# Optimization experiments

Hardware: AMD Instinct MI355X
Metric: run time of the kernel (lower is better)

Reference implementation:

```python
import jax, jax.numpy as jnp
import numpy as np

N, E, D, L, G = 100000, 300000, 256, 5, 4096


def _bn(x, p):
    # p: [4, dim] = (gamma, beta, running_mean, running_var); eval-mode BatchNorm1d
    g, b, m, v = p
    return (x - m) * jax.lax.rsqrt(v + 1e-5) * g + b


def setup_inputs() -> dict:
    key = jax.random.key(0)
    ks = iter(jax.random.split(key, 48))

    def nrm(shape, scale=0.02):
        return jax.random.normal(next(ks), shape, dtype=jnp.float32) * scale

    def bn_params(n, dim):
        g = 1.0 + nrm((n, dim), 0.1)
        b = nrm((n, dim), 0.1)
        m = nrm((n, dim), 0.1)
        v = 1.0 + jax.random.uniform(next(ks), (n, dim), dtype=jnp.float32)
        return jnp.stack([g, b, m, v], axis=1)  # [n,4,dim]

    return {
        "x": jax.random.randint(next(ks), (N, 9), 0, 2, dtype=jnp.int32),
        "edge_index": jax.random.randint(next(ks), (2, E), 0, N, dtype=jnp.int32),
        "edge_attr": jax.random.randint(next(ks), (E, 3), 0, 2, dtype=jnp.int32),
        "batch": jnp.sort(jax.random.randint(next(ks), (N,), 0, G, dtype=jnp.int32)),
        "atom_emb": nrm((9, 120, D)),            # AtomEncoder: 9 feature tables
        "bond_emb": nrm((L, 3, 6, D)),           # per-layer BondEncoder: 3 feature tables
        "vn0": jnp.zeros((D,), jnp.float32),     # virtualnode embedding (init 0)
        "eps": jnp.zeros((L,), jnp.float32),     # GIN eps per layer
        "conv_W1": nrm((L, D, 2 * D), 1.0 / np.sqrt(D)),     # GIN MLP (sampled BayesLinear)
        "conv_b1": nrm((L, 2 * D)),
        "conv_bn1": bn_params(L, 2 * D),
        "conv_W2": nrm((L, 2 * D, D), 1.0 / np.sqrt(2 * D)),
        "conv_b2": nrm((L, D)),
        "node_bn": bn_params(L, D),              # per-layer outer BatchNorm
        "vn_W1": nrm((L - 1, D, D), 1.0 / np.sqrt(D)),       # virtual-node MLP
        "vn_b1": nrm((L - 1, D)),
        "vn_bn1": bn_params(L - 1, D),
        "vn_W2": nrm((L - 1, D, D), 1.0 / np.sqrt(D)),
        "vn_b2": nrm((L - 1, D)),
        "vn_bn2": bn_params(L - 1, D),
    }


def reference(x, edge_index, edge_attr, batch, atom_emb, bond_emb, vn0, eps,
              conv_W1, conv_b1, conv_bn1, conv_W2, conv_b2, node_bn,
              vn_W1, vn_b1, vn_bn1, vn_W2, vn_b2, vn_bn2):
    src, dst = edge_index[0], edge_index[1]
    n_nodes = x.shape[0]
    n_layers = conv_W1.shape[0]
    # AtomEncoder: sum of 9 feature embeddings -> [N, D]
    h = atom_emb[jnp.arange(9), x].sum(axis=1)
    vn = jnp.broadcast_to(vn0, (G, vn0.shape[0]))  # [G, D]
    for l in range(n_layers):
        # broadcast virtual node into graph's nodes
        h = h + vn[batch]
        # GINConv: msg = relu(x_j + bond_emb), sum-aggregate, MLP((1+eps)x + aggr)
        e = bond_emb[l][jnp.arange(3), edge_attr].sum(axis=1)  # [E, D]
        msg = jax.nn.relu(h[src] + e)
        aggr = jax.ops.segment_sum(msg, dst, num_segments=n_nodes)
        t = (1.0 + eps[l]) * h + aggr
        t = jax.nn.relu(_bn(t @ conv_W1[l] + conv_b1[l], conv_bn1[l])) @ conv_W2[l] + conv_b2[l]
        hn = _bn(t, node_bn[l])  # outer BatchNorm (eval); dropout is identity in eval
        if l < n_layers - 1:
            hn = jax.nn.relu(hn)
            # global_add_pool of pre-conv h, then virtual-node MLP update
            vtemp = jax.ops.segment_sum(h, batch, num_segments=G) + vn
            u = jax.nn.relu(_bn(vtemp @ vn_W1[l] + vn_b1[l], vn_bn1[l]))
            vn = jax.nn.relu(_bn(u @ vn_W2[l] + vn_b2[l], vn_bn2[l]))
        h = hn
    return h  # JK == 'last'
```

## Files before the change

kernel.cpp:

```cpp
#include <hip/hip_runtime.h>

#define NN 100000
#define EE 300000
#define DD 256
#define LL 5
#define GG 4096
#define DB 512
#define MPAD 100096

typedef __attribute__((ext_vector_type(4))) float f32x4;
typedef __attribute__((ext_vector_type(8))) short s16x8;

__device__ __forceinline__ ushort f2bf(float f) {
  unsigned u = __float_as_uint(f);
  return (ushort)((u + 0x7fffu + ((u >> 16) & 1u)) >> 16);
}
__device__ __forceinline__ float b2f(ushort u) {
  return __uint_as_float(((unsigned)u) << 16);
}

__device__ __forceinline__ void gload16(const void* g, void* l) {
  __builtin_amdgcn_global_load_lds((const __attribute__((address_space(1))) void*)g,
                                   (__attribute__((address_space(3))) void*)l, 16, 0, 0);
}

__global__ void k_atom(const int* __restrict__ x, const float* __restrict__ emb,
                       const float* __restrict__ vn0, ushort* __restrict__ hvb) {
  int n = blockIdx.x * 4 + (threadIdx.x >> 6);
  if (n >= NN) return;
  int d = (threadIdx.x & 63) * 4;
  const float4 v0 = *(const float4*)&vn0[d];
  float ax = v0.x, ay = v0.y, az = v0.z, aw = v0.w;
#pragma unroll
  for (int f = 0; f < 9; ++f) {
    int v = x[n * 9 + f];
    const float4 t = *(const float4*)&emb[((size_t)(f * 120 + v)) * DD + d];
    ax += t.x; ay += t.y; az += t.z; aw += t.w;
  }
  ushort4 o; o.x = f2bf(ax); o.y = f2bf(ay); o.z = f2bf(az); o.w = f2bf(aw);
  *(ushort4*)&hvb[(size_t)n * DD + d] = o;
}

__global__ void k_vninit(const float* __restrict__ vn0, float* __restrict__ vn) {
  int i = blockIdx.x * blockDim.x + threadIdx.x;
  if (i < GG * DD) vn[i] = vn0[i & (DD - 1)];
}

__global__ void k_goff(const int* __restrict__ batch, int* __restrict__ goff) {
  int g = blockIdx.x * blockDim.x + threadIdx.x;
  if (g > GG) return;
  if (g == GG) { goff[GG] = NN; return; }
  int lo = 0, hi = NN;
  while (lo < hi) { int mid = (lo + hi) >> 1; if (batch[mid] < g) lo = mid + 1; else hi = mid; }
  goff[g] = lo;
}

__global__ void k_zero(int* __restrict__ p, int n) {
  int i = blockIdx.x * 256 + threadIdx.x;
  if (i < n) p[i] = 0;
}

__global__ void k_deg(const int* __restrict__ dst, int* __restrict__ deg) {
  int e = blockIdx.x * 256 + threadIdx.x;
  if (e < EE) atomicAdd(&deg[dst[e]], 1);
}

__global__ void k_scan1(const int* __restrict__ deg, int* __restrict__ coff,
                        int* __restrict__ bsum) {
  __shared__ int wsum[16];
  __shared__ int wpre[16];
  int lane = threadIdx.x & 63, wid = threadIdx.x >> 6;
  int i = blockIdx.x * 1024 + threadIdx.x;
  int v = (i < NN) ? deg[i] : 0;
  int xv = v;
#pragma unroll
  for (int off = 1; off < 64; off <<= 1) {
    int y = __shfl_up(xv, off);
    if (lane >= off) xv += y;
  }
  if (lane == 63) wsum[wid] = xv;
  __syncthreads();
  if (wid == 0 && lane < 16) {
    int s = wsum[lane];
    int xx = s;
#pragma unroll
    for (int off = 1; off < 16; off <<= 1) {
      int y = __shfl_up(xx, off);
      if (lane >= off) xx += y;
    }
    wpre[lane] = xx - s;
  }
  __syncthreads();
  int val = xv + wpre[wid];
  if (i < NN) coff[i + 1] = val;
  if (threadIdx.x == 1023) bsum[blockIdx.x] = val;
}

__global__ void k_scan2(int* __restrict__ bsum, int nb) {
  __shared__ int ws[2];
  int t = threadIdx.x, lane = t & 63, wid = t >> 6;
  int v = (t < nb) ? bsum[t] : 0;
  int xv = v;
#pragma unroll
  for (int off = 1; off < 64; off <<= 1) {
    int y = __shfl_up(xv, off);
    if (lane >= off) xv += y;
  }
  if (lane == 63) ws[wid] = xv;
  __syncthreads();
  int incl = xv + ((wid == 1) ? ws[0] : 0);
  if (t < nb) bsum[t] = incl - v;
}

__global__ void k_scan3(int* __restrict__ coff, const int* __restrict__ bpre) {
  int i = blockIdx.x * 1024 + threadIdx.x;
  if (i == 0) coff[0] = 0;
  if (i < NN) coff[i + 1] += bpre[i >> 10];
}

__global__ void k_eposinit(const int* __restrict__ coff, int* __restrict__ epos) {
  int n = blockIdx.x * 256 + threadIdx.x;
  if (n < NN) epos[n] = coff[n];
}

__global__ void k_scatter(const int* __restrict__ dst, int* __restrict__ epos,
                          int* __restrict__ eid) {
  int e = blockIdx.x * 256 + threadIdx.x;
  if (e < EE) { int p = atomicAdd(&epos[dst[e]], 1); eid[p] = e; }
}

__global__ void k_sort(const int* __restrict__ coff, int* __restrict__ eid) {
  int n = blockIdx.x * 256 + threadIdx.x;
  if (n >= NN) return;
  int s = coff[n], t = coff[n + 1];
  for (int i = s + 1; i < t; ++i) {
    int key = eid[i]; int j = i - 1;
    while (j >= s && eid[j] > key) { eid[j + 1] = eid[j]; --j; }
    eid[j + 1] = key;
  }
}

__global__ void k_emeta(const int* __restrict__ eid, const int* __restrict__ srcs,
                        const int* __restrict__ eattr, unsigned* __restrict__ emeta) {
  int idx = blockIdx.x * 256 + threadIdx.x;
  if (idx >= EE) return;
  int e = eid[idx];
  int s = srcs[e];
  unsigned c = (unsigned)(eattr[e * 3 + 0] + 2 * eattr[e * 3 + 1] + 4 * eattr[e * 3 + 2]);
  emeta[idx] = (unsigned)s | (c << 17);
}

__global__ void k_bond8(const float* __restrict__ bondE, float* __restrict__ bond8) {
  int l = blockIdx.x, c = blockIdx.y, d = threadIdx.x;
  float v = bondE[(((size_t)l * 3 + 0) * 6 + (c & 1)) * DD + d]
          + bondE[(((size_t)l * 3 + 1) * 6 + ((c >> 1) & 1)) * DD + d]
          + bondE[(((size_t)l * 3 + 2) * 6 + ((c >> 2) & 1)) * DD + d];
  bond8[((size_t)l * 8 + c) * DD + d] = v;
}

__global__ void k_wt(const float* __restrict__ in, ushort* __restrict__ out, int K, int N) {
  __shared__ float t[16][17];
  int l = blockIdx.z;
  int kb = blockIdx.x * 16, nb = blockIdx.y * 16;
  int tx = threadIdx.x & 15, ty = threadIdx.x >> 4;
  t[ty][tx] = in[(size_t)l * K * N + (size_t)(kb + ty) * N + nb + tx];
  __syncthreads();
  out[(size_t)l * N * K + (size_t)(nb + ty) * K + kb + tx] = f2bf(t[tx][ty]);
}

__global__ void k_pool(const ushort* __restrict__ hvb, const float* __restrict__ vn,
                       ushort* __restrict__ vtempb, const int* __restrict__ goff) {
  int g = blockIdx.x * 4 + (threadIdx.x >> 6);
  if (g >= GG) return;
  int d = (threadIdx.x & 63) * 4;
  float4 v = *(const float4*)&vn[(size_t)g * DD + d];
  float ax = v.x, ay = v.y, az = v.z, aw = v.w;
  int r0 = goff[g], r1 = goff[g + 1];
  for (int r = r0; r < r1; ++r) {
    ushort4 hu = *(const ushort4*)&hvb[(size_t)r * DD + d];
    ax += b2f(hu.x); ay += b2f(hu.y); az += b2f(hu.z); aw += b2f(hu.w);
  }
  ushort4 o; o.x = f2bf(ax); o.y = f2bf(ay); o.z = f2bf(az); o.w = f2bf(aw);
  *(ushort4*)&vtempb[(size_t)g * DD + d] = o;
}

__global__ void k_aggr(const ushort* __restrict__ hvb, ushort* __restrict__ tb,
                       const unsigned* __restrict__ emeta, const int* __restrict__ coff,
                       const float* __restrict__ bond8l, const float* __restrict__ epsp,
                       int l) {
  int n = blockIdx.x * 4 + (threadIdx.x >> 6);
  if (n >= NN) return;
  int d = (threadIdx.x & 63) * 4;
  float ax = 0.f, ay = 0.f, az = 0.f, aw = 0.f;
  int s0 = coff[n], s1 = coff[n + 1];
  int idx = s0;
  for (; idx + 2 <= s1; idx += 2) {
    unsigned m0 = emeta[idx], m1 = emeta[idx + 1];
    const ushort4 h0 = *(const ushort4*)&hvb[(size_t)(m0 & 0x1FFFFu) * DD + d];
    const ushort4 h1 = *(const ushort4*)&hvb[(size_t)(m1 & 0x1FFFFu) * DD + d];
    const float4 b0 = *(const float4*)&bond8l[(size_t)(m0 >> 17) * DD + d];
    const float4 b1 = *(const float4*)&bond8l[(size_t)(m1 >> 17) * DD + d];
    ax += fmaxf(b2f(h0.x) + b0.x, 0.f) + fmaxf(b2f(h1.x) + b1.x, 0.f);
    ay += fmaxf(b2f(h0.y) + b0.y, 0.f) + fmaxf(b2f(h1.y) + b1.y, 0.f);
    az += fmaxf(b2f(h0.z) + b0.z, 0.f) + fmaxf(b2f(h1.z) + b1.z, 0.f);
    aw += fmaxf(b2f(h0.w) + b0.w, 0.f) + fmaxf(b2f(h1.w) + b1.w, 0.f);
  }
  if (idx < s1) {
    unsigned m0 = emeta[idx];
    const ushort4 h0 = *(const ushort4*)&hvb[(size_t)(m0 & 0x1FFFFu) * DD + d];
    const float4 b0 = *(const float4*)&bond8l[(size_t)(m0 >> 17) * DD + d];
    ax += fmaxf(b2f(h0.x) + b0.x, 0.f);
    ay += fmaxf(b2f(h0.y) + b0.y, 0.f);
    az += fmaxf(b2f(h0.z) + b0.z, 0.f);
    aw += fmaxf(b2f(h0.w) + b0.w, 0.f);
  }
  float ep = 1.f + epsp[l];
  const ushort4 hn = *(const ushort4*)&hvb[(size_t)n * DD + d];
  ushort4 o;
  o.x = f2bf(ep * b2f(hn.x) + ax); o.y = f2bf(ep * b2f(hn.y) + ay);
  o.z = f2bf(ep * b2f(hn.z) + az); o.w = f2bf(ep * b2f(hn.w) + aw);
  *(ushort4*)&tb[(size_t)n * DD + d] = o;
}

__global__ __launch_bounds__(256) void k_mfma_gemm(
    const ushort* __restrict__ A, int M, int K,
    const ushort* __restrict__ BT, int N, int CT,
    void* __restrict__ Cv, int outBf16, int doRelu,
    const float* __restrict__ bias, const float* __restrict__ bn,
    const float* __restrict__ vnAdd, const int* __restrict__ batchv) {
  __shared__ ushort Asm[2][128 * 32];
  __shared__ ushort Bsm[2][128 * 32];
  const int T = gridDim.x;
  const int q = T >> 3, r = T & 7;
  const int xcd = blockIdx.x & 7, li = blockIdx.x >> 3;
  const int w0 = xcd * q + (xcd < r ? xcd : r) + li;
  const int rowBase = (w0 / CT) * 128;
  const int colBase = (w0 % CT) * 128;

  const int tid = threadIdx.x;
  const int lane = tid & 63;
  const int wv = tid >> 6;
  const int wrow = (wv >> 1) * 64, wcol = (wv & 1) * 64;
  const int r16 = lane & 15, kgrp = lane >> 4;

  f32x4 acc[4][4];
#pragma unroll
  for (int m = 0; m < 4; ++m)
#pragma unroll
    for (int n = 0; n < 4; ++n) acc[m][n] = (f32x4)0.f;

  const int ca0 = tid, ca1 = tid + 256;
  const int ra0 = ca0 >> 2, ka0 = (ca0 & 3) ^ ((ra0 >> 1) & 3);
  const int ra1 = ca1 >> 2, ka1 = (ca1 & 3) ^ ((ra1 >> 1) & 3);
  const ushort* Ap0 = A + (size_t)(rowBase + ra0) * K + ka0 * 8;
  const ushort* Ap1 = A + (size_t)(rowBase + ra1) * K + ka1 * 8;
  const ushort* Bp0 = BT + (size_t)(colBase + ra0) * K + ka0 * 8;
  const ushort* Bp1 = BT + (size_t)(colBase + ra1) * K + ka1 * 8;

  int aoff[4], boff[4];
#pragma unroll
  for (int m = 0; m < 4; ++m) {
    int row = wrow + m * 16 + r16;
    aoff[m] = row * 64 + ((kgrp ^ ((row >> 1) & 3)) << 4);
    int col = wcol + m * 16 + r16;
    boff[m] = col * 64 + ((kgrp ^ ((col >> 1) & 3)) << 4);
  }

  const int nk = K >> 5;
  gload16(Ap0, (char*)Asm + ca0 * 16);
  gload16(Ap1, (char*)Asm + ca1 * 16);
  gload16(Bp0, (char*)Bsm + ca0 * 16);
  gload16(Bp1, (char*)Bsm + ca1 * 16);
  __syncthreads();

  int cur = 0;
  for (int t = 0; t < nk; ++t) {
    int nxt = cur ^ 1;
    if (t + 1 < nk) {
      int ko = (t + 1) << 5;
      gload16(Ap0 + ko, (char*)Asm + nxt * 8192 + ca0 * 16);
      gload16(Ap1 + ko, (char*)Asm + nxt * 8192 + ca1 * 16);
      gload16(Bp0 + ko, (char*)Bsm + nxt * 8192 + ca0 * 16);
      gload16(Bp1 + ko, (char*)Bsm + nxt * 8192 + ca1 * 16);
    }
    const char* cA = (const char*)Asm + cur * 8192;
    const char* cB = (const char*)Bsm + cur * 8192;
    s16x8 a[4], b[4];
#pragma unroll
    for (int m = 0; m < 4; ++m) a[m] = *(const s16x8*)(cA + aoff[m]);
#pragma unroll
    for (int n = 0; n < 4; ++n) b[n] = *(const s16x8*)(cB + boff[n]);
#pragma unroll
    for (int m = 0; m < 4; ++m)
#pragma unroll
      for (int n = 0; n < 4; ++n)
        acc[m][n] = __builtin_amdgcn_mfma_f32_16x16x32_bf16(a[m], b[n], acc[m][n], 0, 0, 0);
    __syncthreads();
    cur = nxt;
  }

  float alpha[4], beta[4];
#pragma unroll
  for (int n = 0; n < 4; ++n) {
    int col = colBase + wcol + n * 16 + r16;
    float g = bn[col], bb = bn[N + col], mm = bn[2 * N + col], vv = bn[3 * N + col];
    float s = g * rsqrtf(vv + 1e-5f);
    alpha[n] = s; beta[n] = fmaf(bias[col] - mm, s, bb);
  }
#pragma unroll
  for (int m = 0; m < 4; ++m) {
#pragma unroll
    for (int rr = 0; rr < 4; ++rr) {
      int row = rowBase + wrow + m * 16 + kgrp * 4 + rr;
      if (row < M) {
        const float* vp = vnAdd ? (vnAdd + (size_t)batchv[row] * N) : nullptr;
#pragma unroll
        for (int n = 0; n < 4; ++n) {
          int col = colBase + wcol + n * 16 + r16;
          float v = fmaf(acc[m][n][rr], alpha[n], beta[n]);
          if (doRelu) v = fmaxf(v, 0.f);
          if (vp) v += vp[col];
          if (outBf16) ((ushort*)Cv)[(size_t)row * N + col] = f2bf(v);
          else         ((float*)Cv)[(size_t)row * N + col] = v;
        }
      }
    }
  }
}

extern "C" void kernel_launch(void* const* d_in, const int* in_sizes, int n_in,
                              void* d_out, int out_size, void* d_ws, size_t ws_size,
                              hipStream_t stream) {
  const int*   x     = (const int*)d_in[0];
  const int*   ei    = (const int*)d_in[1];
  const int*   ea    = (const int*)d_in[2];
  const int*   batch = (const int*)d_in[3];
  const float* atomE = (const float*)d_in[4];
  const float* bondE = (const float*)d_in[5];
  const float* vn0   = (const float*)d_in[6];
  const float* eps   = (const float*)d_in[7];
  const float* cW1   = (const float*)d_in[8];
  const float* cb1   = (const float*)d_in[9];
  const float* cbn1  = (const float*)d_in[10];
  const float* cW2   = (const float*)d_in[11];
  const float* cb2   = (const float*)d_in[12];
  const float* nbn   = (const float*)d_in[13];
  const float* vW1   = (const float*)d_in[14];
  const float* vb1   = (const float*)d_in[15];
  const float* vbn1  = (const float*)d_in[16];
  const float* vW2   = (const float*)d_in[17];
  const float* vb2   = (const float*)d_in[18];
  const float* vbn2  = (const float*)d_in[19];
  (void)in_sizes; (void)n_in; (void)out_size; (void)ws_size;

  char* wsp = (char*)d_ws;
  size_t o = 0;
  auto alloc = [&](size_t bytes) -> char* {
    char* p = wsp + o; o += (bytes + 255) & ~(size_t)255; return p;
  };
  ushort* tbuf  = (ushort*)alloc((size_t)MPAD * DD * 2);
  ushort* c1b   = (ushort*)alloc((size_t)MPAD * DB * 2);
  float*  vn    = (float*) alloc((size_t)GG * DD * 4);
  ushort* vtmpb = (ushort*)alloc((size_t)GG * DD * 2);
  ushort* ub    = (ushort*)alloc((size_t)GG * DD * 2);
  ushort* bw1   = (ushort*)alloc((size_t)LL * DB * DD * 2);
  ushort* bw2   = (ushort*)alloc((size_t)LL * DD * DB * 2);
  ushort* bvw1  = (ushort*)alloc((size_t)(LL - 1) * DD * DD * 2);
  ushort* bvw2  = (ushort*)alloc((size_t)(LL - 1) * DD * DD * 2);
  float*  bond8 = (float*) alloc((size_t)LL * 8 * DD * 4);
  unsigned* emeta = (unsigned*)alloc((size_t)EE * 4);
  int* coff = (int*)alloc((size_t)(NN + 1) * 4);
  int* deg  = (int*)alloc((size_t)NN * 4);
  int* epos = (int*)alloc((size_t)NN * 4);
  int* eid  = (int*)alloc((size_t)EE * 4);
  int* goff = (int*)alloc((size_t)(GG + 1) * 4);
  int* bsum = (int*)alloc((size_t)128 * 4);

  const int* srcs = ei;
  const int* dsts = ei + EE;
  ushort* hvb = (ushort*)d_out;

  k_atom<<<(NN + 3) / 4, 256, 0, stream>>>(x, atomE, vn0, hvb);
  k_vninit<<<(GG * DD + 255) / 256, 256, 0, stream>>>(vn0, vn);
  k_goff<<<(GG + 256) / 256, 256, 0, stream>>>(batch, goff);
  k_zero<<<(NN + 255) / 256, 256, 0, stream>>>(deg, NN);
  k_deg<<<(EE + 255) / 256, 256, 0, stream>>>(dsts, deg);
  {
    int nb = (NN + 1023) / 1024;
    k_scan1<<<nb, 1024, 0, stream>>>(deg, coff, bsum);
    k_scan2<<<1, 128, 0, stream>>>(bsum, nb);
    k_scan3<<<nb, 1024, 0, stream>>>(coff, bsum);
  }
  k_eposinit<<<(NN + 255) / 256, 256, 0, stream>>>(coff, epos);
  k_scatter<<<(EE + 255) / 256, 256, 0, stream>>>(dsts, epos, eid);
  k_sort<<<(NN + 255) / 256, 256, 0, stream>>>(coff, eid);
  k_emeta<<<(EE + 255) / 256, 256, 0, stream>>>(eid, srcs, ea, emeta);
  k_bond8<<<dim3(LL, 8), 256, 0, stream>>>(bondE, bond8);
  k_wt<<<dim3(DD / 16, DB / 16, LL), 256, 0, stream>>>(cW1, bw1, DD, DB);
  k_wt<<<dim3(DB / 16, DD / 16, LL), 256, 0, stream>>>(cW2, bw2, DB, DD);
  k_wt<<<dim3(DD / 16, DD / 16, LL - 1), 256, 0, stream>>>(vW1, bvw1, DD, DD);
  k_wt<<<dim3(DD / 16, DD / 16, LL - 1), 256, 0, stream>>>(vW2, bvw2, DD, DD);

  for (int l = 0; l < LL; ++l) {
    if (l < LL - 1) {
      k_pool<<<(GG + 3) / 4, 256, 0, stream>>>(hvb, vn, vtmpb, goff);
      k_mfma_gemm<<<(GG / 128) * 2, 256, 0, stream>>>(
          vtmpb, GG, DD, bvw1 + (size_t)l * DD * DD, DD, 2,
          ub, 1, 1, vb1 + (size_t)l * DD, vbn1 + (size_t)l * 4 * DD, nullptr, nullptr);
      k_mfma_gemm<<<(GG / 128) * 2, 256, 0, stream>>>(
          ub, GG, DD, bvw2 + (size_t)l * DD * DD, DD, 2,
          vn, 0, 1, vb2 + (size_t)l * DD, vbn2 + (size_t)l * 4 * DD, nullptr, nullptr);
    }
    k_aggr<<<(NN + 3) / 4, 256, 0, stream>>>(hvb, tbuf, emeta, coff,
                                             bond8 + (size_t)l * 8 * DD, eps, l);
    k_mfma_gemm<<<(MPAD / 128) * 4, 256, 0, stream>>>(
        tbuf, NN, DD, bw1 + (size_t)l * DB * DD, DB, 4,
        c1b, 1, 1, cb1 + (size_t)l * DB, cbn1 + (size_t)l * 4 * DB, nullptr, nullptr);
    if (l < LL - 1) {
      k_mfma_gemm<<<(MPAD / 128) * 2, 256, 0, stream>>>(
          c1b, NN, DB, bw2 + (size_t)l * DD * DB, DD, 2,
          hvb, 1, 1, cb2 + (size_t)l * DD, nbn + (size_t)l * 4 * DD, vn, batch);
    } else {
      k_mfma_gemm<<<(MPAD / 128) * 2, 256, 0, stream>>>(
          c1b, NN, DB, bw2 + (size_t)l * DD * DB, DD, 2,
          (float*)d_out, 0, 0, cb2 + (size_t)l * DD, nbn + (size_t)l * 4 * DD,
          nullptr, nullptr);
    }
  }
}
```

Before: 1.160 ms.

## Triple-buffer GEMM LDS tiles with explicit vmcnt waits and single barrier

Moves the bf16 MFMA GEMM from double to triple buffering in LDS. Loads are issued two K-steps ahead, and explicit s_waitcnt vmcnt counts replace the full drain, leaving one barrier per iteration instead of two. It also raises wave priority around the MFMA block. The aim is to hide global-to-LDS load latency better, at the cost of 50% more LDS per block, which may reduce occupancy. Correctness depends on the hand-coded vmcnt values matching the four loads issued per stage.

After: 1.170 ms. No clear change (+0.9%).

```diff
diff --git a/kernel.cpp b/kernel.cpp
--- a/kernel.cpp
+++ b/kernel.cpp
@@ -228,8 +228,8 @@
     void* __restrict__ Cv, int outBf16, int doRelu,
     const float* __restrict__ bias, const float* __restrict__ bn,
     const float* __restrict__ vnAdd, const int* __restrict__ batchv) {
-  __shared__ ushort Asm[2][128 * 32];
-  __shared__ ushort Bsm[2][128 * 32];
+  __shared__ ushort Asm[3][128 * 32];
+  __shared__ ushort Bsm[3][128 * 32];
   const int T = gridDim.x;
   const int q = T >> 3, r = T & 7;
   const int xcd = blockIdx.x & 7, li = blockIdx.x >> 3;
@@ -267,36 +267,37 @@
   }
 
   const int nk = K >> 5;
-  gload16(Ap0, (char*)Asm + ca0 * 16);
-  gload16(Ap1, (char*)Asm + ca1 * 16);
-  gload16(Bp0, (char*)Bsm + ca0 * 16);
-  gload16(Bp1, (char*)Bsm + ca1 * 16);
-  __syncthreads();
-
-  int cur = 0;
+  auto stage = [&](int t) {
+    int b = t % 3;
+    int ko = t << 5;
+    gload16(Ap0 + ko, (char*)Asm[b] + ca0 * 16);
+    gload16(Ap1 + ko, (char*)Asm[b] + ca1 * 16);
+    gload16(Bp0 + ko, (char*)Bsm[b] + ca0 * 16);
+    gload16(Bp1 + ko, (char*)Bsm[b] + ca1 * 16);
+  };
+  stage(0);
+  if (nk > 1) stage(1);
+
   for (int t = 0; t < nk; ++t) {
-    int nxt = cur ^ 1;
-    if (t + 1 < nk) {
-      int ko = (t + 1) << 5;
-      gload16(Ap0 + ko, (char*)Asm + nxt * 8192 + ca0 * 16);
-      gload16(Ap1 + ko, (char*)Asm + nxt * 8192 + ca1 * 16);
-      gload16(Bp0 + ko, (char*)Bsm + nxt * 8192 + ca0 * 16);
-      gload16(Bp1 + ko, (char*)Bsm + nxt * 8192 + ca1 * 16);
-    }
-    const char* cA = (const char*)Asm + cur * 8192;
-    const char* cB = (const char*)Bsm + cur * 8192;
+    if (t + 1 < nk) asm volatile("s_waitcnt vmcnt(4)" ::: "memory");
+    else            asm volatile("s_waitcnt vmcnt(0)" ::: "memory");
+    __builtin_amdgcn_s_barrier();
+    __builtin_amdgcn_sched_barrier(0);
+    if (t + 2 < nk) stage(t + 2);
+    const char* cA = (const char*)Asm[t % 3];
+    const char* cB = (const char*)Bsm[t % 3];
     s16x8 a[4], b[4];
 #pragma unroll
     for (int m = 0; m < 4; ++m) a[m] = *(const s16x8*)(cA + aoff[m]);
 #pragma unroll
     for (int n = 0; n < 4; ++n) b[n] = *(const s16x8*)(cB + boff[n]);
+    __builtin_amdgcn_s_setprio(1);
 #pragma unroll
     for (int m = 0; m < 4; ++m)
 #pragma unroll
       for (int n = 0; n < 4; ++n)
         acc[m][n] = __builtin_amdgcn_mfma_f32_16x16x32_bf16(a[m], b[n], acc[m][n], 0, 0, 0);
-    __syncthreads();
-    cur = nxt;
+    __builtin_amdgcn_s_setprio(0);
   }
 
   float alpha[4], beta[4];
```

## Double GEMM K-tile to 64 and use a 2D grid for the second conv GEMM

Applied to the files above, without the earlier changes.

The MFMA GEMM now stages 64-wide K slices per iteration instead of 32, with a new 8-way XOR swizzle. Each iteration issues two MFMA sub-steps, so the number of barriers and loop iterations is halved. A remap flag is added so the second conv GEMM can launch on a plain 2D grid with row/col taken from blockIdx, bypassing the XCD-aware remapping. LDS use per block doubles to 64 KB, which may reduce occupancy.

Result: slower. 1.311 ms (+13.0%).

```diff
diff --git a/kernel.cpp b/kernel.cpp
--- a/kernel.cpp
+++ b/kernel.cpp
@@ -224,19 +224,24 @@
 
 __global__ __launch_bounds__(256) void k_mfma_gemm(
     const ushort* __restrict__ A, int M, int K,
-    const ushort* __restrict__ BT, int N, int CT,
+    const ushort* __restrict__ BT, int N, int CT, int remap,
     void* __restrict__ Cv, int outBf16, int doRelu,
     const float* __restrict__ bias, const float* __restrict__ bn,
     const float* __restrict__ vnAdd, const int* __restrict__ batchv) {
-  __shared__ ushort Asm[2][128 * 32];
-  __shared__ ushort Bsm[2][128 * 32];
-  const int T = gridDim.x;
-  const int q = T >> 3, r = T & 7;
-  const int xcd = blockIdx.x & 7, li = blockIdx.x >> 3;
-  const int w0 = xcd * q + (xcd < r ? xcd : r) + li;
-  const int rowBase = (w0 / CT) * 128;
-  const int colBase = (w0 % CT) * 128;
-
+  __shared__ ushort Asm[2][128 * 64];
+  __shared__ ushort Bsm[2][128 * 64];
+  int rowBase, colBase;
+  if (remap) {
+    const int T = gridDim.x;
+    const int q = T >> 3, r = T & 7;
+    const int xcd = blockIdx.x & 7, li = blockIdx.x >> 3;
+    const int w0 = xcd * q + (xcd < r ? xcd : r) + li;
+    rowBase = (w0 / CT) * 128;
+    colBase = (w0 % CT) * 128;
+  } else {
+    rowBase = blockIdx.x * 128;
+    colBase = blockIdx.y * 128;
+  }
   const int tid = threadIdx.x;
   const int lane = tid & 63;
   const int wv = tid >> 6;
@@ -249,54 +254,61 @@
 #pragma unroll
     for (int n = 0; n < 4; ++n) acc[m][n] = (f32x4)0.f;
 
-  const int ca0 = tid, ca1 = tid + 256;
-  const int ra0 = ca0 >> 2, ka0 = (ca0 & 3) ^ ((ra0 >> 1) & 3);
-  const int ra1 = ca1 >> 2, ka1 = (ca1 & 3) ^ ((ra1 >> 1) & 3);
-  const ushort* Ap0 = A + (size_t)(rowBase + ra0) * K + ka0 * 8;
-  const ushort* Ap1 = A + (size_t)(rowBase + ra1) * K + ka1 * 8;
-  const ushort* Bp0 = BT + (size_t)(colBase + ra0) * K + ka0 * 8;
-  const ushort* Bp1 = BT + (size_t)(colBase + ra1) * K + ka1 * 8;
-
-  int aoff[4], boff[4];
+  const ushort* Ap[4];
+  const ushort* Bp[4];
+#pragma unroll
+  for (int i = 0; i < 4; ++i) {
+    int c = tid + i * 256;
+    int row = c >> 3, kg = (c & 7) ^ (row & 7);
+    Ap[i] = A + (size_t)(rowBase + row) * K + kg * 8;
+    Bp[i] = BT + (size_t)(colBase + row) * K + kg * 8;
+  }
+
+  int aoff[4][2], boff[4][2];
 #pragma unroll
   for (int m = 0; m < 4; ++m) {
     int row = wrow + m * 16 + r16;
-    aoff[m] = row * 64 + ((kgrp ^ ((row >> 1) & 3)) << 4);
     int col = wcol + m * 16 + r16;
-    boff[m] = col * 64 + ((kgrp ^ ((col >> 1) & 3)) << 4);
-  }
-
-  const int nk = K >> 5;
-  gload16(Ap0, (char*)Asm + ca0 * 16);
-  gload16(Ap1, (char*)Asm + ca1 * 16);
-  gload16(Bp0, (char*)Bsm + ca0 * 16);
-  gload16(Bp1, (char*)Bsm + ca1 * 16);
+#pragma unroll
+    for (int ks = 0; ks < 2; ++ks) {
+      aoff[m][ks] = row * 128 + (((ks * 4 + kgrp) ^ (row & 7)) << 4);
+      boff[m][ks] = col * 128 + (((ks * 4 + kgrp) ^ (col & 7)) << 4);
+    }
+  }
+
+  const int nk = K >> 6;
+  auto stage = [&](int t, int b) {
+    int ko = t << 6;
+#pragma unroll
+    for (int i = 0; i < 4; ++i)
+      gload16(Ap[i] + ko, (char*)Asm[b] + (tid + i * 256) * 16);
+#pragma unroll
+    for (int i = 0; i < 4; ++i)
+      gload16(Bp[i] + ko, (char*)Bsm[b] + (tid + i * 256) * 16);
+  };
+
+  stage(0, 0);
   __syncthreads();
-
   int cur = 0;
   for (int t = 0; t < nk; ++t) {
-    int nxt = cur ^ 1;
-    if (t + 1 < nk) {
-      int ko = (t + 1) << 5;
-      gload16(Ap0 + ko, (char*)Asm + nxt * 8192 + ca0 * 16);
-      gload16(Ap1 + ko, (char*)Asm + nxt * 8192 + ca1 * 16);
-      gload16(Bp0 + ko, (char*)Bsm + nxt * 8192 + ca0 * 16);
-      gload16(Bp1 + ko, (char*)Bsm + nxt * 8192 + ca1 * 16);
-    }
-    const char* cA = (const char*)Asm + cur * 8192;
-    const char* cB = (const char*)Bsm + cur * 8192;
-    s16x8 a[4], b[4];
-#pragma unroll
-    for (int m = 0; m < 4; ++m) a[m] = *(const s16x8*)(cA + aoff[m]);
-#pragma unroll
-    for (int n = 0; n < 4; ++n) b[n] = *(const s16x8*)(cB + boff[n]);
-#pragma unroll
-    for (int m = 0; m < 4; ++m)
-#pragma unroll
-      for (int n = 0; n < 4; ++n)
-        acc[m][n] = __builtin_amdgcn_mfma_f32_16x16x32_bf16(a[m], b[n], acc[m][n], 0, 0, 0);
+    if (t + 1 < nk) stage(t + 1, cur ^ 1);
+    const char* cA = (const char*)Asm[cur];
+    const char* cB = (const char*)Bsm[cur];
+#pragma unroll
+    for (int ks = 0; ks < 2; ++ks) {
+      s16x8 a[4], b[4];
+#pragma unroll
+      for (int m = 0; m < 4; ++m) a[m] = *(const s16x8*)(cA + aoff[m][ks]);
+#pragma unroll
+      for (int n = 0; n < 4; ++n) b[n] = *(const s16x8*)(cB + boff[n][ks]);
+#pragma unroll
+      for (int m = 0; m < 4; ++m)
+#pragma unroll
+        for (int n = 0; n < 4; ++n)
+          acc[m][n] = __builtin_amdgcn_mfma_f32_16x16x32_bf16(a[m], b[n], acc[m][n], 0, 0, 0);
+    }
     __syncthreads();
-    cur = nxt;
+    cur ^= 1;
   }
 
   float alpha[4], beta[4];
@@ -405,24 +417,24 @@
     if (l < LL - 1) {
       k_pool<<<(GG + 3) / 4, 256, 0, stream>>>(hvb, vn, vtmpb, goff);
       k_mfma_gemm<<<(GG / 128) * 2, 256, 0, stream>>>(
-          vtmpb, GG, DD, bvw1 + (size_t)l * DD * DD, DD, 2,
+          vtmpb, GG, DD, bvw1 + (size_t)l * DD * DD, DD, 2, 1,
           ub, 1, 1, vb1 + (size_t)l * DD, vbn1 + (size_t)l * 4 * DD, nullptr, nullptr);
       k_mfma_gemm<<<(GG / 128) * 2, 256, 0, stream>>>(
-          ub, GG, DD, bvw2 + (size_t)l * DD * DD, DD, 2,
+          ub, GG, DD, bvw2 + (size_t)l * DD * DD, DD, 2, 1,
           vn, 0, 1, vb2 + (size_t)l * DD, vbn2 + (size_t)l * 4 * DD, nullptr, nullptr);
     }
     k_aggr<<<(NN + 3) / 4, 256, 0, stream>>>(hvb, tbuf, emeta, coff,
                                              bond8 + (size_t)l * 8 * DD, eps, l);
     k_mfma_gemm<<<(MPAD / 128) * 4, 256, 0, stream>>>(
-        tbuf, NN, DD, bw1 + (size_t)l * DB * DD, DB, 4,
+        tbuf, NN, DD, bw1 + (size_t)l * DB * DD, DB, 4, 1,
         c1b, 1, 1, cb1 + (size_t)l * DB, cbn1 + (size_t)l * 4 * DB, nullptr, nullptr);
     if (l < LL - 1) {
-      k_mfma_gemm<<<(MPAD / 128) * 2, 256, 0, stream>>>(
-          c1b, NN, DB, bw2 + (size_t)l * DD * DB, DD, 2,
+      k_mfma_gemm<<<dim3(MPAD / 128, DD / 128), 256, 0, stream>>>(
+          c1b, NN, DB, bw2 + (size_t)l * DD * DB, DD, 0, 0,
           hvb, 1, 1, cb2 + (size_t)l * DD, nbn + (size_t)l * 4 * DD, vn, batch);
     } else {
-      k_mfma_gemm<<<(MPAD / 128) * 2, 256, 0, stream>>>(
-          c1b, NN, DB, bw2 + (size_t)l * DD * DB, DD, 2,
+      k_mfma_gemm<<<dim3(MPAD / 128, DD / 128), 256, 0, stream>>>(
+          c1b, NN, DB, bw2 + (size_t)l * DD * DB, DD, 0, 0,
           (float*)d_out, 0, 0, cb2 + (size_t)l * DD, nbn + (size_t)l * 4 * DD,
           nullptr, nullptr);
     }
```

## Replace tiled GEMM with weight-stationary kernel keeping full-K B slice in LDS

Applied to the files above, without the earlier changes.

The double-buffered 128x128 LDS-tiled MFMA GEMM is replaced by a templated weight-stationary kernel. Each block loads a 64-column slice of the transposed weight over the full K into swizzled LDS once. Each wave then streams its own 64 rows of A straight from global memory into registers, with no per-k-step barriers. This removes the per-iteration syncs and the A staging through LDS. In exchange, A is re-read once per column tile, global loads are not double-buffered, and LDS use reaches 64KB for K=512, which may lower occupancy.

Result: slower. 1.641 ms (+41.5%).

```diff
diff --git a/kernel.cpp b/kernel.cpp
--- a/kernel.cpp
+++ b/kernel.cpp
@@ -222,26 +222,40 @@
   *(ushort4*)&tb[(size_t)n * DD + d] = o;
 }
 
-__global__ __launch_bounds__(256) void k_mfma_gemm(
-    const ushort* __restrict__ A, int M, int K,
-    const ushort* __restrict__ BT, int N, int CT,
+template<int K>
+__global__ __launch_bounds__(256) void k_gemm_ws(
+    const ushort* __restrict__ A, int M,
+    const ushort* __restrict__ BT, int N,
     void* __restrict__ Cv, int outBf16, int doRelu,
     const float* __restrict__ bias, const float* __restrict__ bn,
     const float* __restrict__ vnAdd, const int* __restrict__ batchv) {
-  __shared__ ushort Asm[2][128 * 32];
-  __shared__ ushort Bsm[2][128 * 32];
-  const int T = gridDim.x;
-  const int q = T >> 3, r = T & 7;
-  const int xcd = blockIdx.x & 7, li = blockIdx.x >> 3;
-  const int w0 = xcd * q + (xcd < r ? xcd : r) + li;
-  const int rowBase = (w0 / CT) * 128;
-  const int colBase = (w0 % CT) * 128;
-
+  constexpr int SL = K / 8;
+  __shared__ ushort Bs[64 * K];
   const int tid = threadIdx.x;
   const int lane = tid & 63;
   const int wv = tid >> 6;
-  const int wrow = (wv >> 1) * 64, wcol = (wv & 1) * 64;
   const int r16 = lane & 15, kgrp = lane >> 4;
+  const int rowBase = blockIdx.x * 256 + wv * 64;
+  const int colBase = blockIdx.y * 64;
+
+#pragma unroll
+  for (int i = 0; i < 64 * SL / 256; ++i) {
+    int c = tid + i * 256;
+    int col = c / SL, sl = c % SL;
+    int kg = sl ^ (col & 7);
+    gload16(BT + (size_t)(colBase + col) * K + kg * 8, (char*)Bs + c * 16);
+  }
+  __syncthreads();
+
+  const ushort* ap[4];
+#pragma unroll
+  for (int m = 0; m < 4; ++m)
+    ap[m] = A + (size_t)(rowBase + m * 16 + r16) * K + kgrp * 8;
+
+  int boff[4];
+#pragma unroll
+  for (int n = 0; n < 4; ++n) boff[n] = (n * 16 + r16) * (2 * K);
+  const int cx7 = r16 & 7;
 
   f32x4 acc[4][4];
 #pragma unroll
@@ -249,60 +263,25 @@
 #pragma unroll
     for (int n = 0; n < 4; ++n) acc[m][n] = (f32x4)0.f;
 
-  const int ca0 = tid, ca1 = tid + 256;
-  const int ra0 = ca0 >> 2, ka0 = (ca0 & 3) ^ ((ra0 >> 1) & 3);
-  const int ra1 = ca1 >> 2, ka1 = (ca1 & 3) ^ ((ra1 >> 1) & 3);
-  const ushort* Ap0 = A + (size_t)(rowBase + ra0) * K + ka0 * 8;
-  const ushort* Ap1 = A + (size_t)(rowBase + ra1) * K + ka1 * 8;
-  const ushort* Bp0 = BT + (size_t)(colBase + ra0) * K + ka0 * 8;
-  const ushort* Bp1 = BT + (size_t)(colBase + ra1) * K + ka1 * 8;
-
-  int aoff[4], boff[4];
-#pragma unroll
-  for (int m = 0; m < 4; ++m) {
-    int row = wrow + m * 16 + r16;
-    aoff[m] = row * 64 + ((kgrp ^ ((row >> 1) & 3)) << 4);
-    int col = wcol + m * 16 + r16;
-    boff[m] = col * 64 + ((kgrp ^ ((col >> 1) & 3)) << 4);
-  }
-
-  const int nk = K >> 5;
-  gload16(Ap0, (char*)Asm + ca0 * 16);
-  gload16(Ap1, (char*)Asm + ca1 * 16);
-  gload16(Bp0, (char*)Bsm + ca0 * 16);
-  gload16(Bp1, (char*)Bsm + ca1 * 16);
-  __syncthreads();
-
-  int cur = 0;
-  for (int t = 0; t < nk; ++t) {
-    int nxt = cur ^ 1;
-    if (t + 1 < nk) {
-      int ko = (t + 1) << 5;
-      gload16(Ap0 + ko, (char*)Asm + nxt * 8192 + ca0 * 16);
-      gload16(Ap1 + ko, (char*)Asm + nxt * 8192 + ca1 * 16);
-      gload16(Bp0 + ko, (char*)Bsm + nxt * 8192 + ca0 * 16);
-      gload16(Bp1 + ko, (char*)Bsm + nxt * 8192 + ca1 * 16);
-    }
-    const char* cA = (const char*)Asm + cur * 8192;
-    const char* cB = (const char*)Bsm + cur * 8192;
+#pragma unroll 4
+  for (int t = 0; t < K / 32; ++t) {
     s16x8 a[4], b[4];
 #pragma unroll
-    for (int m = 0; m < 4; ++m) a[m] = *(const s16x8*)(cA + aoff[m]);
-#pragma unroll
-    for (int n = 0; n < 4; ++n) b[n] = *(const s16x8*)(cB + boff[n]);
+    for (int m = 0; m < 4; ++m) a[m] = *(const s16x8*)(ap[m] + t * 32);
+    const int so = (((t * 4 + kgrp) ^ cx7) << 4);
+#pragma unroll
+    for (int n = 0; n < 4; ++n) b[n] = *(const s16x8*)((const char*)Bs + boff[n] + so);
 #pragma unroll
     for (int m = 0; m < 4; ++m)
 #pragma unroll
       for (int n = 0; n < 4; ++n)
         acc[m][n] = __builtin_amdgcn_mfma_f32_16x16x32_bf16(a[m], b[n], acc[m][n], 0, 0, 0);
-    __syncthreads();
-    cur = nxt;
   }
 
   float alpha[4], beta[4];
 #pragma unroll
   for (int n = 0; n < 4; ++n) {
-    int col = colBase + wcol + n * 16 + r16;
+    int col = colBase + n * 16 + r16;
     float g = bn[col], bb = bn[N + col], mm = bn[2 * N + col], vv = bn[3 * N + col];
     float s = g * rsqrtf(vv + 1e-5f);
     alpha[n] = s; beta[n] = fmaf(bias[col] - mm, s, bb);
@@ -311,12 +290,12 @@
   for (int m = 0; m < 4; ++m) {
 #pragma unroll
     for (int rr = 0; rr < 4; ++rr) {
-      int row = rowBase + wrow + m * 16 + kgrp * 4 + rr;
+      int row = rowBase + m * 16 + kgrp * 4 + rr;
       if (row < M) {
         const float* vp = vnAdd ? (vnAdd + (size_t)batchv[row] * N) : nullptr;
 #pragma unroll
         for (int n = 0; n < 4; ++n) {
-          int col = colBase + wcol + n * 16 + r16;
+          int col = colBase + n * 16 + r16;
           float v = fmaf(acc[m][n][rr], alpha[n], beta[n]);
           if (doRelu) v = fmaxf(v, 0.f);
           if (vp) v += vp[col];
@@ -404,25 +383,25 @@
   for (int l = 0; l < LL; ++l) {
     if (l < LL - 1) {
       k_pool<<<(GG + 3) / 4, 256, 0, stream>>>(hvb, vn, vtmpb, goff);
-      k_mfma_gemm<<<(GG / 128) * 2, 256, 0, stream>>>(
-          vtmpb, GG, DD, bvw1 + (size_t)l * DD * DD, DD, 2,
+      k_gemm_ws<256><<<dim3(GG / 256, DD / 64), 256, 0, stream>>>(
+          vtmpb, GG, bvw1 + (size_t)l * DD * DD, DD,
           ub, 1, 1, vb1 + (size_t)l * DD, vbn1 + (size_t)l * 4 * DD, nullptr, nullptr);
-      k_mfma_gemm<<<(GG / 128) * 2, 256, 0, stream>>>(
-          ub, GG, DD, bvw2 + (size_t)l * DD * DD, DD, 2,
+      k_gemm_ws<256><<<dim3(GG / 256, DD / 64), 256, 0, stream>>>(
+          ub, GG, bvw2 + (size_t)l * DD * DD, DD,
           vn, 0, 1, vb2 + (size_t)l * DD, vbn2 + (size_t)l * 4 * DD, nullptr, nullptr);
     }
     k_aggr<<<(NN + 3) / 4, 256, 0, stream>>>(hvb, tbuf, emeta, coff,
                                              bond8 + (size_t)l * 8 * DD, eps, l);
-    k_mfma_gemm<<<(MPAD / 128) * 4, 256, 0, stream>>>(
-        tbuf, NN, DD, bw1 + (size_t)l * DB * DD, DB, 4,
+    k_gemm_ws<256><<<dim3(MPAD / 256, DB / 64), 256, 0, stream>>>(
+        tbuf, NN, bw1 + (size_t)l * DB * DD, DB,
         c1b, 1, 1, cb1 + (size_t)l * DB, cbn1 + (size_t)l * 4 * DB, nullptr, nullptr);
     if (l < LL - 1) {
-      k_mfma_gemm<<<(MPAD / 128) * 2, 256, 0, stream>>>(
-          c1b, NN, DB, bw2 + (size_t)l * DD * DB, DD, 2,
+      k_gemm_ws<512><<<dim3(MPAD / 256, DD / 64), 256, 0, stream>>>(
+          c1b, NN, bw2 + (size_t)l * DD * DB, DD,
           hvb, 1, 1, cb2 + (size_t)l * DD, nbn + (size_t)l * 4 * DD, vn, batch);
     } else {
-      k_mfma_gemm<<<(MPAD / 128) * 2, 256, 0, stream>>>(
-          c1b, NN, DB, bw2 + (size_t)l * DD * DB, DD, 2,
+      k_gemm_ws<512><<<dim3(MPAD / 256, DD / 64), 256, 0, stream>>>(
+          c1b, NN, bw2 + (size_t)l * DD * DB, DD,
           (float*)d_out, 0, 0, cb2 + (size_t)l * DD, nbn + (size_t)l * 4 * DD,
           nullptr, nullptr);
     }
```
